# Optimization experiments

Measured on AMD Instinct MI355X. Metric: run time of the kernel, lower is better.

## Reference

```python
import jax, jax.numpy as jnp
import numpy as np

NUM_BINS = 32
EPS = 1e-8


def setup_inputs() -> dict:
    key = jax.random.key(0)
    k1, k2, k3 = jax.random.split(key, 3)
    H, W = 4096, 4096
    return {
        "stu_tensor": jax.random.uniform(k1, (H, W), dtype=jnp.float32),
        "tea_tensor": jax.random.uniform(k2, (H, W), dtype=jnp.float32),
        "stu_uncertainty": jax.random.uniform(k3, (H, W), dtype=jnp.float32),
    }


def reference(stu_tensor, tea_tensor, stu_uncertainty):
    # topo consistency and confidence maps, both in [0, 1]
    topo = 1.0 - jnp.abs(stu_tensor - tea_tensor)
    conf = 1.0 - stu_uncertainty

    # --- mutual information via 2D joint histogram (single bucketize + scatter-add) ---
    bins = jnp.linspace(0.0, 1.0, NUM_BINS + 1)
    # torch loop uses [bins[i], bins[i+1]) half-open intervals -> searchsorted 'right' - 1
    ti = jnp.searchsorted(bins, topo.ravel(), side="right") - 1
    ci = jnp.searchsorted(bins, conf.ravel(), side="right") - 1
    valid = (ti >= 0) & (ti < NUM_BINS) & (ci >= 0) & (ci < NUM_BINS)
    ti_c = jnp.clip(ti, 0, NUM_BINS - 1)
    ci_c = jnp.clip(ci, 0, NUM_BINS - 1)
    joint_hist = jnp.zeros((NUM_BINS, NUM_BINS), dtype=jnp.float32).at[ti_c, ci_c].add(
        valid.astype(jnp.float32)
    )
    total = joint_hist.sum()
    joint_prob = joint_hist / (total + EPS)
    marg_topo = joint_prob.sum(axis=1)  # (NUM_BINS,)
    marg_conf = joint_prob.sum(axis=0)  # (NUM_BINS,)
    mi_terms = joint_prob * jnp.log(
        joint_prob / (marg_topo[:, None] * marg_conf[None, :] + EPS) + EPS
    )
    mi = jnp.where(joint_prob > EPS, mi_terms, 0.0).sum()
    mi = jnp.where(total < EPS, 0.0, mi)
    mi_loss = -mi

    # --- conditional entropy over high-confidence pixels ---
    high_conf = conf > 0.8
    cnt = high_conf.sum()
    topo_clamp = jnp.clip(topo, EPS, 1.0 - EPS)
    ent_map = -(topo_clamp * jnp.log(topo_clamp + EPS))
    masked_mean = (ent_map * high_conf).sum() / jnp.maximum(cnt, 1).astype(jnp.float32)
    entropy_loss = jnp.where(cnt > 10, masked_mean, 0.0)

    return mi_loss + 0.1 * entropy_loss
```

## Files before the change

### kernel.cpp

```cpp
#include <hip/hip_runtime.h>
#include <math.h>

#define NBINS 32
#define NB2   1024
#define EPSD  1e-8


__device__ inline double block_reduce_sum_d(double v, double* sh) {
#pragma unroll
    for (int o = 32; o > 0; o >>= 1) v += __shfl_down(v, o, 64);
    const int lane = threadIdx.x & 63;
    const int wave = threadIdx.x >> 6;
    const int nw   = blockDim.x >> 6;
    __syncthreads();
    if (lane == 0) sh[wave] = v;
    __syncthreads();
    double r = (threadIdx.x < nw) ? sh[threadIdx.x] : 0.0;
    if (wave == 0) {
#pragma unroll
        for (int o = 8; o > 0; o >>= 1) r += __shfl_down(r, o, 64);
    }
    return r;
}

extern "C" __global__ void __launch_bounds__(1024)
topo_zero_kernel(unsigned int* __restrict__ ghist,
                 double* __restrict__ gent,
                 unsigned int* __restrict__ gcnt)
{
    ghist[threadIdx.x] = 0u;
    if (threadIdx.x == 0) { *gent = 0.0; *gcnt = 0u; }
}

__device__ inline void process4(float4 s, float4 t, float4 u,
                                unsigned int* myh, float& ent, unsigned int& cnt)
{
    float sv[4] = {s.x, s.y, s.z, s.w};
    float tv[4] = {t.x, t.y, t.z, t.w};
    float uv[4] = {u.x, u.y, u.z, u.w};
#pragma unroll
    for (int k = 0; k < 4; ++k) {
        float topo = 1.0f - fabsf(sv[k] - tv[k]);
        float conf = 1.0f - uv[k];
        int ti = (int)(topo * 32.0f);
        int ci = (int)(conf * 32.0f);
        if (ti < NBINS && ci < NBINS)
            atomicAdd(&myh[(ti << 5) + ci], 1u);
        bool hc = conf > 0.8f;
        float tc = fminf(fmaxf(topo, 1e-8f), 1.0f - 1e-8f);
        float e  = -tc * __logf(tc + 1e-8f);
        ent += hc ? e : 0.0f;
        cnt += hc ? 1u : 0u;
    }
}

extern "C" __global__ void __launch_bounds__(256)
topo_hist_kernel(const float* __restrict__ stu, const float* __restrict__ tea,
                 const float* __restrict__ unc,
                 unsigned int* __restrict__ ghist,
                 double* __restrict__ gent,
                 unsigned int* __restrict__ gcnt,
                 int n)
{
    __shared__ unsigned int sh_hist[4 * NB2];
    __shared__ double sh_red[4];

    const int wave = threadIdx.x >> 6;
    unsigned int* myh = sh_hist + wave * NB2;

    for (int i = threadIdx.x; i < 4 * NB2; i += blockDim.x) sh_hist[i] = 0u;
    __syncthreads();

    float ent = 0.0f;
    unsigned int cnt = 0;

    const int n4     = n >> 2;
    const int gid    = blockIdx.x * blockDim.x + threadIdx.x;
    const int stride = gridDim.x * blockDim.x;

    const float4* s4 = (const float4*)stu;
    const float4* t4 = (const float4*)tea;
    const float4* u4 = (const float4*)unc;

    int i = gid;
    for (; i + stride < n4; i += 2 * stride) {
        float4 s0 = s4[i];          float4 s1 = s4[i + stride];
        float4 t0 = t4[i];          float4 t1 = t4[i + stride];
        float4 u0 = u4[i];          float4 u1 = u4[i + stride];
        process4(s0, t0, u0, myh, ent, cnt);
        process4(s1, t1, u1, myh, ent, cnt);
    }
    for (; i < n4; i += stride) {
        process4(s4[i], t4[i], u4[i], myh, ent, cnt);
    }
    for (int j = (n4 << 2) + gid; j < n; j += stride) {
        float topo = 1.0f - fabsf(stu[j] - tea[j]);
        float conf = 1.0f - unc[j];
        int ti = (int)(topo * 32.0f);
        int ci = (int)(conf * 32.0f);
        if (ti < NBINS && ci < NBINS)
            atomicAdd(&myh[(ti << 5) + ci], 1u);
        if (conf > 0.8f) {
            float tc = fminf(fmaxf(topo, 1e-8f), 1.0f - 1e-8f);
            ent += -tc * __logf(tc + 1e-8f);
            cnt++;
        }
    }

    __syncthreads();
    for (int b = threadIdx.x; b < NB2; b += blockDim.x) {
        unsigned int v = sh_hist[b] + sh_hist[NB2 + b] +
                         sh_hist[2 * NB2 + b] + sh_hist[3 * NB2 + b];
        if (v) atomicAdd(&ghist[b], v);
    }

    double es = block_reduce_sum_d((double)ent, sh_red);
    double cs = block_reduce_sum_d((double)cnt, sh_red);
    if (threadIdx.x == 0) {
        atomicAdd(gent, es);
        atomicAdd(gcnt, (unsigned int)(cs + 0.5));
    }
}

extern "C" __global__ void __launch_bounds__(1024)
topo_final_kernel(const unsigned int* __restrict__ ghist,
                  const double* __restrict__ gent,
                  const unsigned int* __restrict__ gcnt,
                  float* __restrict__ out)
{
    __shared__ double sh_red[16];
    __shared__ double jp[NB2];
    __shared__ double marg_r[NBINS];
    __shared__ double marg_c[NBINS];
    __shared__ double bcast;

    const int tid = threadIdx.x;

    double dc = (double)ghist[tid];

    double total = block_reduce_sum_d(dc, sh_red);
    if (tid == 0) bcast = total;
    __syncthreads();
    total = bcast;

    double p = dc / (total + EPSD);
    jp[tid] = p;
    __syncthreads();

    if (tid < NBINS) {
        double s = 0.0;
        for (int cc = 0; cc < NBINS; ++cc) s += jp[(tid << 5) + cc];
        marg_r[tid] = s;
    } else if (tid < 2 * NBINS) {
        int cc = tid - NBINS;
        double s = 0.0;
        for (int r = 0; r < NBINS; ++r) s += jp[(r << 5) + cc];
        marg_c[cc] = s;
    }
    __syncthreads();

    const int r  = tid >> 5;
    const int cc = tid & 31;
    double term = 0.0;
    if (p > EPSD)
        term = p * log(p / (marg_r[r] * marg_c[cc] + EPSD) + EPSD);
    double mi = block_reduce_sum_d(term, sh_red);

    if (tid == 0) {
        double es = *gent;
        double cs = (double)(*gcnt);
        double mi_v     = (total < EPSD) ? 0.0 : mi;
        double mean     = es / fmax(cs, 1.0);
        double ent_loss = (cs > 10.0) ? mean : 0.0;
        out[0] = (float)(-mi_v + 0.1 * ent_loss);
    }
}

extern "C" void kernel_launch(void* const* d_in, const int* in_sizes, int n_in,
                              void* d_out, int out_size, void* d_ws, size_t ws_size,
                              hipStream_t stream) {
    const float* stu = (const float*)d_in[0];
    const float* tea = (const float*)d_in[1];
    const float* unc = (const float*)d_in[2];
    float* out = (float*)d_out;
    int n = in_sizes[0];

    unsigned int* ghist = (unsigned int*)d_ws;
    double*       gent  = (double*)((char*)d_ws + 4096);
    unsigned int* gcnt  = (unsigned int*)((char*)d_ws + 4104);

    const int B = 2048;

    topo_zero_kernel<<<1, 1024, 0, stream>>>(ghist, gent, gcnt);
    topo_hist_kernel<<<B, 256, 0, stream>>>(stu, tea, unc, ghist, gent, gcnt, n);
    topo_final_kernel<<<1, 1024, 0, stream>>>(ghist, gent, gcnt, out);
}
```

Baseline: 218.2 us.

## Replace global histogram atomics with per-block partials and a two-stage reduction

Each block now writes its full 1024-bin histogram, entropy sum and count to its own workspace slot instead of doing global atomics. A new reduce kernel folds the block partials into 32 intermediate histograms, and the final kernel sums those along with the per-block entropy and count values. This removes the zeroing kernel and the contention of many blocks hitting the same 1024 global addresses. The grid also shrinks from 2048 to 1024 blocks, and the streaming loop is unrolled to four strides. The cost is extra workspace traffic and one more launch; workspace offsets stay fixed even when the block count is reduced for a small workspace.

```diff
diff --git a/kernel.cpp b/kernel.cpp
--- a/kernel.cpp
+++ b/kernel.cpp
@@ -4,7 +4,13 @@
 #define NBINS 32
 #define NB2   1024
 #define EPSD  1e-8
-
+#define MAXB  1024
+
+
+#define OFF_P2   (MAXB * NB2 * sizeof(unsigned int))
+#define OFF_ENT  (OFF_P2 + 32 * NB2 * sizeof(unsigned int))
+#define OFF_CNT  (OFF_ENT + MAXB * sizeof(double))
+#define WS_NEED  (OFF_CNT + MAXB * sizeof(unsigned int))
 
 __device__ inline double block_reduce_sum_d(double v, double* sh) {
 #pragma unroll
@@ -21,15 +27,6 @@
         for (int o = 8; o > 0; o >>= 1) r += __shfl_down(r, o, 64);
     }
     return r;
-}
-
-extern "C" __global__ void __launch_bounds__(1024)
-topo_zero_kernel(unsigned int* __restrict__ ghist,
-                 double* __restrict__ gent,
-                 unsigned int* __restrict__ gcnt)
-{
-    ghist[threadIdx.x] = 0u;
-    if (threadIdx.x == 0) { *gent = 0.0; *gcnt = 0u; }
 }
 
 __device__ inline void process4(float4 s, float4 t, float4 u,
@@ -57,9 +54,9 @@
 extern "C" __global__ void __launch_bounds__(256)
 topo_hist_kernel(const float* __restrict__ stu, const float* __restrict__ tea,
                  const float* __restrict__ unc,
-                 unsigned int* __restrict__ ghist,
-                 double* __restrict__ gent,
-                 unsigned int* __restrict__ gcnt,
+                 unsigned int* __restrict__ hist_part,
+                 double* __restrict__ ent_part,
+                 unsigned int* __restrict__ cnt_part,
                  int n)
 {
     __shared__ unsigned int sh_hist[4 * NB2];
@@ -83,16 +80,18 @@
     const float4* u4 = (const float4*)unc;
 
     int i = gid;
-    for (; i + stride < n4; i += 2 * stride) {
-        float4 s0 = s4[i];          float4 s1 = s4[i + stride];
-        float4 t0 = t4[i];          float4 t1 = t4[i + stride];
-        float4 u0 = u4[i];          float4 u1 = u4[i + stride];
+    for (; i + 3 * stride < n4; i += 4 * stride) {
+        float4 s0 = s4[i];              float4 t0 = t4[i];              float4 u0 = u4[i];
+        float4 s1 = s4[i + stride];     float4 t1 = t4[i + stride];     float4 u1 = u4[i + stride];
+        float4 s2 = s4[i + 2 * stride]; float4 t2 = t4[i + 2 * stride]; float4 u2 = u4[i + 2 * stride];
+        float4 s3 = s4[i + 3 * stride]; float4 t3 = t4[i + 3 * stride]; float4 u3 = u4[i + 3 * stride];
         process4(s0, t0, u0, myh, ent, cnt);
         process4(s1, t1, u1, myh, ent, cnt);
-    }
-    for (; i < n4; i += stride) {
+        process4(s2, t2, u2, myh, ent, cnt);
+        process4(s3, t3, u3, myh, ent, cnt);
+    }
+    for (; i < n4; i += stride)
         process4(s4[i], t4[i], u4[i], myh, ent, cnt);
-    }
     for (int j = (n4 << 2) + gid; j < n; j += stride) {
         float topo = 1.0f - fabsf(stu[j] - tea[j]);
         float conf = 1.0f - unc[j];
@@ -111,22 +110,37 @@
     for (int b = threadIdx.x; b < NB2; b += blockDim.x) {
         unsigned int v = sh_hist[b] + sh_hist[NB2 + b] +
                          sh_hist[2 * NB2 + b] + sh_hist[3 * NB2 + b];
-        if (v) atomicAdd(&ghist[b], v);
+        hist_part[(size_t)blockIdx.x * NB2 + b] = v;
     }
 
     double es = block_reduce_sum_d((double)ent, sh_red);
     double cs = block_reduce_sum_d((double)cnt, sh_red);
     if (threadIdx.x == 0) {
-        atomicAdd(gent, es);
-        atomicAdd(gcnt, (unsigned int)(cs + 0.5));
-    }
+        ent_part[blockIdx.x] = es;
+        cnt_part[blockIdx.x] = cs;
+    }
+    if (threadIdx.x == 0) cnt_part[blockIdx.x] = (unsigned int)(cs + 0.5);
+}
+
+extern "C" __global__ void __launch_bounds__(256)
+topo_reduce_kernel(const unsigned int* __restrict__ hist_part,
+                   unsigned int* __restrict__ partial2, int B)
+{
+    const int g   = blockIdx.x;
+    const int s   = g >> 2;
+    const int c   = g & 3;
+    const int bin = (c << 8) + threadIdx.x;
+    unsigned int acc = 0;
+    for (int b = s; b < B; b += 32)
+        acc += hist_part[(size_t)b * NB2 + bin];
+    partial2[s * NB2 + bin] = acc;
 }
 
 extern "C" __global__ void __launch_bounds__(1024)
-topo_final_kernel(const unsigned int* __restrict__ ghist,
-                  const double* __restrict__ gent,
-                  const unsigned int* __restrict__ gcnt,
-                  float* __restrict__ out)
+topo_final_kernel(const unsigned int* __restrict__ partial2,
+                  const double* __restrict__ ent_part,
+                  const unsigned int* __restrict__ cnt_part,
+                  int B, float* __restrict__ out)
 {
     __shared__ double sh_red[16];
     __shared__ double jp[NB2];
@@ -136,7 +150,10 @@
 
     const int tid = threadIdx.x;
 
-    double dc = (double)ghist[tid];
+    unsigned int c = 0;
+#pragma unroll
+    for (int s = 0; s < 32; ++s) c += partial2[s * NB2 + tid];
+    double dc = (double)c;
 
     double total = block_reduce_sum_d(dc, sh_red);
     if (tid == 0) bcast = total;
@@ -166,9 +183,12 @@
         term = p * log(p / (marg_r[r] * marg_c[cc] + EPSD) + EPSD);
     double mi = block_reduce_sum_d(term, sh_red);
 
+    double ev = (tid < B) ? ent_part[tid] : 0.0;
+    double es = block_reduce_sum_d(ev, sh_red);
+    double cv = (tid < B) ? (double)cnt_part[tid] : 0.0;
+    double cs = block_reduce_sum_d(cv, sh_red);
+
     if (tid == 0) {
-        double es = *gent;
-        double cs = (double)(*gcnt);
         double mi_v     = (total < EPSD) ? 0.0 : mi;
         double mean     = es / fmax(cs, 1.0);
         double ent_loss = (cs > 10.0) ? mean : 0.0;
@@ -185,13 +205,21 @@
     float* out = (float*)d_out;
     int n = in_sizes[0];
 
-    unsigned int* ghist = (unsigned int*)d_ws;
-    double*       gent  = (double*)((char*)d_ws + 4096);
-    unsigned int* gcnt  = (unsigned int*)((char*)d_ws + 4104);
-
-    const int B = 2048;
-
-    topo_zero_kernel<<<1, 1024, 0, stream>>>(ghist, gent, gcnt);
-    topo_hist_kernel<<<B, 256, 0, stream>>>(stu, tea, unc, ghist, gent, gcnt, n);
-    topo_final_kernel<<<1, 1024, 0, stream>>>(ghist, gent, gcnt, out);
-}
+    int B = MAXB;
+    if (ws_size < WS_NEED) {
+        size_t per = NB2 * sizeof(unsigned int);
+        size_t fixed = 32 * NB2 * sizeof(unsigned int) + MAXB * (sizeof(double) + sizeof(unsigned int));
+        B = (ws_size > fixed) ? (int)((ws_size - fixed) / per) : 1;
+        if (B < 1) B = 1;
+        if (B > MAXB) B = MAXB;
+    }
+
+    unsigned int* hist_part = (unsigned int*)d_ws;
+    unsigned int* partial2  = (unsigned int*)((char*)d_ws + OFF_P2);
+    double*       ent_part  = (double*)((char*)d_ws + OFF_ENT);
+    unsigned int* cnt_part  = (unsigned int*)((char*)d_ws + OFF_CNT);
+
+    topo_hist_kernel<<<B, 256, 0, stream>>>(stu, tea, unc, hist_part, ent_part, cnt_part, n);
+    topo_reduce_kernel<<<128, 256, 0, stream>>>(hist_part, partial2, B);
+    topo_final_kernel<<<1, 1024, 0, stream>>>(partial2, ent_part, cnt_part, B, out);
+}
```

After: 212.0 us. 2.8% less time.
